# Performance work log

Hardware: AMD Instinct MI355X
Metric: run time of the kernel (lower is better)

Reference implementation:

```python
import jax, jax.numpy as jnp
import numpy as np

WEIGHT = 1.0
BOND_CUTOFF = 2.4


def setup_inputs() -> dict:
    key = jax.random.key(0)
    k0, k1, k2, k3, k4, k5 = jax.random.split(key, 6)
    N_TOK, L, B = 512, 3072, 2
    is_ligand = jax.random.randint(k0, (N_TOK,), 0, 2) > 0
    token_bonds = jax.random.randint(k1, (N_TOK, N_TOK), 0, 2) > 0
    atom_to_token_map = jax.random.randint(k2, (L,), 0, N_TOK, dtype=jnp.int32)
    crd_mask_L = jax.random.randint(k3, (B, L), 0, 2) > 0
    X_L = jax.random.normal(k4, (B, L, 3), dtype=jnp.float32)
    X_gt_L = jax.random.normal(k5, (B, L, 3), dtype=jnp.float32)
    return {
        'is_ligand': is_ligand,
        'token_bonds': token_bonds,
        'atom_to_token_map': atom_to_token_map,
        'crd_mask_L': crd_mask_L,
        'X_L': X_L,
        'X_gt_L': X_gt_L,
    }


def _pairwise_sqdist(X):
    # X: [B, L, 3] -> [B, L, L] squared pairwise distances
    d = X[:, :, None, :] - X[:, None, :, :]
    return jnp.sum(d * d, axis=-1)


def reference(is_ligand, token_bonds, atom_to_token_map, crd_mask_L, X_L, X_gt_L):
    # inter-polymer-ligand token pair mask: ligand i, non-ligand j
    inter = is_ligand[:, None] & (~is_ligand)[None, :]          # [T, T]
    pl_bonds = token_bonds & inter                              # [T, T]
    # The original O(n_bonds * L^2) loop is exactly this gather:
    pl_atoms = pl_bonds[atom_to_token_map[:, None], atom_to_token_map[None, :]]  # [L, L]
    crd_mask_LL = crd_mask_L[:, :, None] & crd_mask_L[:, None, :]                # [B, L, L]
    mask = pl_atoms[None, :, :] & crd_mask_LL                                    # [B, L, L]

    # safe sqrt (masked entries set to 1 before sqrt; excluded from loss anyway)
    pred = jnp.sqrt(jnp.where(mask, _pairwise_sqdist(X_L), 1.0))
    gt = jnp.sqrt(jnp.where(mask, _pairwise_sqdist(X_gt_L), 1.0))

    bonded = mask & (gt < BOND_CUTOFF)
    err2 = jnp.where(bonded, jnp.square(pred - gt), 0.0)
    cnt = jnp.maximum(jnp.sum(bonded), 1)
    loss = jnp.sum(err2) / cnt.astype(err2.dtype)
    return (WEIGHT * loss, loss)
```

## Files before the change

kernel.cpp:

```cpp
#include <hip/hip_runtime.h>

#define L 3072
#define NT 512
#define CUT2 5.76f
#define GRID 256
#define BLOCK 1024

typedef unsigned int u32;
typedef unsigned long long u64;

__global__ __launch_bounds__(BLOCK) void plbl_main(
    const int* __restrict__ is_ligand,
    const int* __restrict__ token_bonds,
    const int* __restrict__ tokmap,
    const int* __restrict__ crd,
    const float* __restrict__ X,
    const float* __restrict__ Xgt,
    double* __restrict__ part_sum,
    u32* __restrict__ part_cnt)
{
    const int t = threadIdx.x;
    const int lane = t & 63;
    const int wv = t >> 6;

    __shared__ u32 s_wtot[2][16];
    __shared__ u32 s_colmeta[3072];
    __shared__ u32 s_rowlist[3072];
    __shared__ u32 s_cnts[2];
    __shared__ u64 s_bond[8];
    __shared__ double s_rsum[16];
    __shared__ u32 s_rcnt[16];

    u32 cc = 0, rc = 0;
    u32 meta[3];
    bool cok[3], rok[3];
    #pragma unroll
    for (int k = 0; k < 3; k++) {
        const int a = t * 3 + k;
        const int tok = tokmap[a];
        const int lig = is_ligand[tok];
        const u32 m0 = crd[a] != 0;
        const u32 m1 = crd[L + a] != 0;
        const bool any = (m0 | m1) != 0u;
        meta[k] = (u32)a | ((u32)tok << 12) | (m0 << 21) | (m1 << 22);
        cok[k] = (lig == 0) && any;
        rok[k] = (lig != 0) && any;
        cc += cok[k] ? 1u : 0u;
        rc += rok[k] ? 1u : 0u;
    }

    u32 ci = cc, ri = rc;
    #pragma unroll
    for (int o = 1; o < 64; o <<= 1) {
        u32 cv = __shfl_up(ci, o, 64);
        u32 rv = __shfl_up(ri, o, 64);
        if (lane >= o) { ci += cv; ri += rv; }
    }
    if (lane == 63) { s_wtot[0][wv] = ci; s_wtot[1][wv] = ri; }
    __syncthreads();

    if (wv == 0 && lane < 16) {
        const u32 c = s_wtot[0][lane];
        const u32 r = s_wtot[1][lane];
        u32 cs = c, rs = r;
        #pragma unroll
        for (int o = 1; o < 16; o <<= 1) {
            u32 cv = __shfl_up(cs, o, 64);
            u32 rv = __shfl_up(rs, o, 64);
            if (lane >= o) { cs += cv; rs += rv; }
        }
        s_wtot[0][lane] = cs - c;
        s_wtot[1][lane] = rs - r;
        if (lane == 15) { s_cnts[0] = cs; s_cnts[1] = rs; }
    }
    __syncthreads();

    u32 coff = s_wtot[0][wv] + (ci - cc);
    u32 roff = s_wtot[1][wv] + (ri - rc);
    #pragma unroll
    for (int k = 0; k < 3; k++) {
        if (cok[k]) s_colmeta[coff++] = meta[k];
        if (rok[k]) s_rowlist[roff++] = meta[k];
    }
    __syncthreads();

    const int ncol = (int)s_cnts[0];
    const int nrow = (int)s_cnts[1];

    double acc = 0.0;
    u32 cnt = 0;

    for (int rb = blockIdx.x; rb < nrow; rb += GRID) {
        const u32 rm = s_rowlist[rb];
        const int a1  = rm & 0xFFF;
        const u32 ta1 = (rm >> 12) & 0x1FF;
        const u32 rbits = (rm >> 21) & 3u;

        if (t < 512) {
            const bool bv = token_bonds[ta1 * NT + t] != 0;
            const u64 bal = __ballot(bv);
            if (lane == 0) s_bond[wv] = bal;
        }
        __syncthreads();

        const float p0x = X[(0 * L + a1) * 3 + 0];
        const float p0y = X[(0 * L + a1) * 3 + 1];
        const float p0z = X[(0 * L + a1) * 3 + 2];
        const float p1x = X[(1 * L + a1) * 3 + 0];
        const float p1y = X[(1 * L + a1) * 3 + 1];
        const float p1z = X[(1 * L + a1) * 3 + 2];
        const float g0x = Xgt[(0 * L + a1) * 3 + 0];
        const float g0y = Xgt[(0 * L + a1) * 3 + 1];
        const float g0z = Xgt[(0 * L + a1) * 3 + 2];
        const float g1x = Xgt[(1 * L + a1) * 3 + 0];
        const float g1y = Xgt[(1 * L + a1) * 3 + 1];
        const float g1z = Xgt[(1 * L + a1) * 3 + 2];

        for (int j = t; j < ncol; j += BLOCK) {
            const u32 cm = s_colmeta[j];
            const int a2 = (int)(cm & 0xFFF);
            const u32 tok = (cm >> 12) & 0x1FF;
            const bool bond = (s_bond[tok >> 6] >> (tok & 63)) & 1ULL;

            const int b0 = 3 * a2;
            const int b1 = 3 * L + 3 * a2;
            const float vx0 = X[b0 + 0], vy0 = X[b0 + 1], vz0 = X[b0 + 2];
            const float vx1 = X[b1 + 0], vy1 = X[b1 + 1], vz1 = X[b1 + 2];
            const float wx0 = Xgt[b0 + 0], wy0 = Xgt[b0 + 1], wz0 = Xgt[b0 + 2];
            const float wx1 = Xgt[b1 + 0], wy1 = Xgt[b1 + 1], wz1 = Xgt[b1 + 2];

            const float dgx0 = g0x - wx0, dgy0 = g0y - wy0, dgz0 = g0z - wz0;
            const float gt2_0 = dgx0 * dgx0 + dgy0 * dgy0 + dgz0 * dgz0;
            const float dpx0 = p0x - vx0, dpy0 = p0y - vy0, dpz0 = p0z - vz0;
            const float pr2_0 = dpx0 * dpx0 + dpy0 * dpy0 + dpz0 * dpz0;
            const float d0 = sqrtf(pr2_0) - sqrtf(gt2_0);
            const bool k0 = bond && (rbits & 1u) && ((cm >> 21) & 1u) && (gt2_0 < CUT2);
            const float dgx1 = g1x - wx1, dgy1 = g1y - wy1, dgz1 = g1z - wz1;
            const float gt2_1 = dgx1 * dgx1 + dgy1 * dgy1 + dgz1 * dgz1;
            const float dpx1 = p1x - vx1, dpy1 = p1y - vy1, dpz1 = p1z - vz1;
            const float pr2_1 = dpx1 * dpx1 + dpy1 * dpy1 + dpz1 * dpz1;
            const float d1 = sqrtf(pr2_1) - sqrtf(gt2_1);
            const bool k1 = bond && (rbits & 2u) && ((cm >> 22) & 1u) && (gt2_1 < CUT2);

            const float e = (k0 ? d0 * d0 : 0.0f) + (k1 ? d1 * d1 : 0.0f);
            acc += (double)e;
            cnt += (k0 ? 1u : 0u) + (k1 ? 1u : 0u);
        }
        __syncthreads();
    }

    #pragma unroll
    for (int o = 32; o > 0; o >>= 1) {
        acc += __shfl_down(acc, o, 64);
        cnt += __shfl_down(cnt, o, 64);
    }
    if (lane == 0) { s_rsum[wv] = acc; s_rcnt[wv] = cnt; }
    __syncthreads();
    if (t == 0) {
        double a = 0.0;
        u32 c = 0;
        #pragma unroll
        for (int i = 0; i < 16; i++) { a += s_rsum[i]; c += s_rcnt[i]; }
        part_sum[blockIdx.x] = a;
        part_cnt[blockIdx.x] = c;
    }
}

__global__ __launch_bounds__(256) void plbl_fin(
    const double* __restrict__ part_sum,
    const u32* __restrict__ part_cnt,
    float* __restrict__ out)
{
    const int t = threadIdx.x;
    const int lane = t & 63;
    const int wv = t >> 6;
    double a = part_sum[t];
    u32 c = part_cnt[t];
    #pragma unroll
    for (int o = 32; o > 0; o >>= 1) {
        a += __shfl_down(a, o, 64);
        c += __shfl_down(c, o, 64);
    }
    __shared__ double s_sum[4];
    __shared__ u32 s_cnt[4];
    if (lane == 0) { s_sum[wv] = a; s_cnt[wv] = c; }
    __syncthreads();
    if (t == 0) {
        const double sum = s_sum[0] + s_sum[1] + s_sum[2] + s_sum[3];
        const u32 cc = s_cnt[0] + s_cnt[1] + s_cnt[2] + s_cnt[3];
        const u32 n = cc ? cc : 1u;
        const float loss = (float)(sum / (double)n);
        out[0] = loss;
        out[1] = loss;
    }
}

extern "C" void kernel_launch(void* const* d_in, const int* in_sizes, int n_in,
                              void* d_out, int out_size, void* d_ws, size_t ws_size,
                              hipStream_t stream) {
    const int*   is_ligand   = (const int*)d_in[0];
    const int*   token_bonds = (const int*)d_in[1];
    const int*   tokmap      = (const int*)d_in[2];
    const int*   crd_mask    = (const int*)d_in[3];
    const float* X           = (const float*)d_in[4];
    const float* Xgt         = (const float*)d_in[5];
    float* out = (float*)d_out;

    char* w = (char*)d_ws;
    double* part_sum = (double*)(w + 0);
    u32*    part_cnt = (u32*)(w + 8 * GRID);

    plbl_main<<<GRID, BLOCK, 0, stream>>>(is_ligand, token_bonds, tokmap,
                                          crd_mask, X, Xgt,
                                          part_sum, part_cnt);
    plbl_fin<<<1, 256, 0, stream>>>(part_sum, part_cnt, out);
}
```

Before: 20.23 us.

## Precompute per-block bond bitmasks and stage ligand flags in shared memory

Is_ligand is loaded once into a shared bitmask instead of gathered per atom. Rows are now assigned to blocks as contiguous chunks, and all bond-row ballots for the block are computed up front into a per-row shared array. This removes the two barriers per row in the main loop and lets the token_bonds loads overlap. If a block gets more than MAXRPB rows (nrow above 3072 cannot happen, but rpb can exceed 12 when nrow exceeds 3072), indexing would overflow. Contiguous chunking also changes how the load is balanced across blocks.

New measurement: 18.65 us. -7.8%, faster.

```diff
diff --git a/kernel.cpp b/kernel.cpp
--- a/kernel.cpp
+++ b/kernel.cpp
@@ -5,6 +5,7 @@
 #define CUT2 5.76f
 #define GRID 256
 #define BLOCK 1024
+#define MAXRPB 12
 
 typedef unsigned int u32;
 typedef unsigned long long u64;
@@ -23,13 +24,21 @@
     const int lane = t & 63;
     const int wv = t >> 6;
 
+    __shared__ u64 s_lig[8];
     __shared__ u32 s_wtot[2][16];
+    __shared__ u32 s_cnts[2];
     __shared__ u32 s_colmeta[3072];
     __shared__ u32 s_rowlist[3072];
-    __shared__ u32 s_cnts[2];
-    __shared__ u64 s_bond[8];
+    __shared__ u64 s_bond[MAXRPB][8];
     __shared__ double s_rsum[16];
     __shared__ u32 s_rcnt[16];
+
+    if (t < NT) {
+        const bool v = is_ligand[t] != 0;
+        const u64 bal = __ballot(v);
+        if (lane == 0) s_lig[wv] = bal;
+    }
+    __syncthreads();
 
     u32 cc = 0, rc = 0;
     u32 meta[3];
@@ -37,14 +46,14 @@
     #pragma unroll
     for (int k = 0; k < 3; k++) {
         const int a = t * 3 + k;
-        const int tok = tokmap[a];
-        const int lig = is_ligand[tok];
+        const u32 tok = (u32)tokmap[a];
+        const bool lig = (s_lig[tok >> 6] >> (tok & 63)) & 1ULL;
         const u32 m0 = crd[a] != 0;
         const u32 m1 = crd[L + a] != 0;
         const bool any = (m0 | m1) != 0u;
-        meta[k] = (u32)a | ((u32)tok << 12) | (m0 << 21) | (m1 << 22);
-        cok[k] = (lig == 0) && any;
-        rok[k] = (lig != 0) && any;
+        meta[k] = (u32)a | (tok << 12) | (m0 << 21) | (m1 << 22);
+        cok[k] = (!lig) && any;
+        rok[k] = lig && any;
         cc += cok[k] ? 1u : 0u;
         rc += rok[k] ? 1u : 0u;
     }
@@ -87,21 +96,29 @@
     const int ncol = (int)s_cnts[0];
     const int nrow = (int)s_cnts[1];
 
+    const int rpb = (nrow + GRID - 1) / GRID;
+    const int r0 = blockIdx.x * rpb;
+    const int r1 = (r0 + rpb < nrow) ? (r0 + rpb) : nrow;
+    const int nr = (r1 > r0) ? (r1 - r0) : 0;
+
+    for (int r = 0; r < nr; r++) {
+        const u32 rm = s_rowlist[r0 + r];
+        const u32 ta1 = (rm >> 12) & 0x1FF;
+        if (t < NT) {
+            const bool bv = token_bonds[ta1 * NT + t] != 0;
+            const u64 bal = __ballot(bv);
+            if (lane == 0) s_bond[r][wv] = bal;
+        }
+    }
+    __syncthreads();
+
     double acc = 0.0;
     u32 cnt = 0;
 
-    for (int rb = blockIdx.x; rb < nrow; rb += GRID) {
-        const u32 rm = s_rowlist[rb];
-        const int a1  = rm & 0xFFF;
-        const u32 ta1 = (rm >> 12) & 0x1FF;
+    for (int r = 0; r < nr; r++) {
+        const u32 rm = s_rowlist[r0 + r];
+        const int a1  = (int)(rm & 0xFFF);
         const u32 rbits = (rm >> 21) & 3u;
-
-        if (t < 512) {
-            const bool bv = token_bonds[ta1 * NT + t] != 0;
-            const u64 bal = __ballot(bv);
-            if (lane == 0) s_bond[wv] = bal;
-        }
-        __syncthreads();
 
         const float p0x = X[(0 * L + a1) * 3 + 0];
         const float p0y = X[(0 * L + a1) * 3 + 1];
@@ -120,7 +137,7 @@
             const u32 cm = s_colmeta[j];
             const int a2 = (int)(cm & 0xFFF);
             const u32 tok = (cm >> 12) & 0x1FF;
-            const bool bond = (s_bond[tok >> 6] >> (tok & 63)) & 1ULL;
+            const bool bond = (s_bond[r][tok >> 6] >> (tok & 63)) & 1ULL;
 
             const int b0 = 3 * a2;
             const int b1 = 3 * L + 3 * a2;
@@ -146,7 +163,6 @@
             acc += (double)e;
             cnt += (k0 ? 1u : 0u) + (k1 ? 1u : 0u);
         }
-        __syncthreads();
     }
 
     #pragma unroll
```
